# Performance work log

Hardware: AMD Instinct MI355X
Metric: run time of the kernel (lower is better)

The kernel has to match this reference:

```python
import jax, jax.numpy as jnp
import numpy as np

HEADS = 16
SCALE = 8.0
EPS = 1e-12  # F.normalize eps for fp32


def _l2norm(t):
    # F.normalize(t, dim=-1): t / max(||t||, eps)
    n = jnp.sqrt(jnp.sum(t * t, axis=-1, keepdims=True))
    return t / jnp.maximum(n, EPS)


def setup_inputs() -> dict:
    key = jax.random.key(0)
    k0, k1, k2, k3, k4 = jax.random.split(key, 5)
    b, n, d = 1, 4096, 1024
    w_scale = 1.0 / np.sqrt(d)
    return {
        "x": jax.random.normal(k0, (b, n, d), dtype=jnp.float32),
        "Wq": jax.random.normal(k1, (d, d), dtype=jnp.float32) * w_scale,
        "Wk": jax.random.normal(k2, (d, d), dtype=jnp.float32) * w_scale,
        "Wv": jax.random.normal(k3, (d, d), dtype=jnp.float32) * w_scale,
        "Wo": jax.random.normal(k4, (d, d), dtype=jnp.float32) * w_scale,
    }


def reference(x, Wq, Wk, Wv, Wo):
    b, n, d = x.shape
    h = HEADS
    dh = d // h
    # projections (nn.Linear without bias): y = x @ W  (W stored as [in, out])
    def proj(W):
        y = jnp.einsum('bnd,df->bnf', x, W)
        return y.reshape(b, n, h, dh).transpose(0, 2, 1, 3)  # b h n dh
    q, k, v = proj(Wq), proj(Wk), proj(Wv)
    # cosine-sim attention: L2-normalize q, k along head dim
    q = _l2norm(q)
    k = _l2norm(k)
    sim = jnp.einsum('bhid,bhjd->bhij', q, k) * SCALE
    mask_value = -jnp.finfo(sim.dtype).max
    causal = jnp.triu(jnp.ones((n, n), dtype=bool), 1)
    sim = jnp.where(causal, mask_value, sim)
    attn = jax.nn.softmax(sim, axis=-1)
    o = jnp.einsum('bhij,bhjd->bhid', attn, v)
    o = o.transpose(0, 2, 1, 3).reshape(b, n, d)  # b n (h dh)
    return jnp.einsum('bnf,fd->bnd', o, Wo)
```

## Files before the change

kernel.cpp:

```cpp
#include <hip/hip_runtime.h>
#include <stdint.h>
#include <math.h>

typedef __bf16 bf16_t;
typedef __attribute__((ext_vector_type(8))) __bf16 bf16x8;
typedef __attribute__((ext_vector_type(4))) __bf16 bf16x4;
typedef __attribute__((ext_vector_type(4))) float f32x4;

#define N_TOK 4096
#define D_MODEL 1024
#define HEADS 16
#define DH 64
#define C1 11.541560327111707f

__device__ __forceinline__ void async_copy16(const void* g, void* l) {
    __builtin_amdgcn_global_load_lds(
        (const __attribute__((address_space(1))) unsigned int*)g,
        (__attribute__((address_space(3))) unsigned int*)l, 16, 0, 0);
}

__global__ __launch_bounds__(256) void cast_x_kernel(const float* __restrict__ x,
                                                     bf16_t* __restrict__ xb) {
    int i = (blockIdx.x * 256 + threadIdx.x) * 4;
    float4 v = *(const float4*)(x + i);
    bf16x4 o;
    o[0] = (bf16_t)v.x; o[1] = (bf16_t)v.y; o[2] = (bf16_t)v.z; o[3] = (bf16_t)v.w;
    *(bf16x4*)(xb + i) = o;
}

__global__ __launch_bounds__(256) void transpose_w_kernel(
    const float* __restrict__ W0, const float* __restrict__ W1,
    const float* __restrict__ W2, const float* __restrict__ W3,
    bf16_t* __restrict__ T0, bf16_t* __restrict__ T1,
    bf16_t* __restrict__ T2, bf16_t* __restrict__ T3) {
    __shared__ bf16_t t[64][72];
    const float* W; bf16_t* T;
    switch (blockIdx.z) {
        case 0: W = W0; T = T0; break;
        case 1: W = W1; T = T1; break;
        case 2: W = W2; T = T2; break;
        default: W = W3; T = T3; break;
    }
    int k0 = blockIdx.x * 64, n0 = blockIdx.y * 64;
    int tx = threadIdx.x & 63, ty = threadIdx.x >> 6;
#pragma unroll
    for (int i = 0; i < 16; i++) {
        int kl = ty * 16 + i;
        t[kl][tx] = (bf16_t)W[(size_t)(k0 + kl) * D_MODEL + n0 + tx];
    }
    __syncthreads();
#pragma unroll
    for (int i = 0; i < 16; i++) {
        int nl = ty * 16 + i;
        T[(size_t)(n0 + nl) * D_MODEL + k0 + tx] = t[tx][nl];
    }
}

template <int WRITE_F32, int NORM>
__global__ __launch_bounds__(256) void gemm_tile(const bf16_t* __restrict__ A,
                                                 const bf16_t* __restrict__ Bt,
                                                 void* __restrict__ Cout, int ldc) {
    constexpr int K = D_MODEL;
    __shared__ __align__(16) bf16_t As[2][128 * 32];
    __shared__ __align__(16) bf16_t Bs[2][128 * 32];
    const int tid = threadIdx.x;
    const int m0 = blockIdx.y * 128;
    const int n0 = blockIdx.x * 128;
    const int wave = tid >> 6;
    const int lane = tid & 63;
    const int l15 = lane & 15;
    const int quad = lane >> 4;
    const int wm = (wave >> 1) * 64;
    const int wn = (wave & 1) * 64;
    f32x4 acc[4][4] = {};

    const int srow = tid >> 2;
    const int soff = (tid & 3) * 8;
    const bf16_t* gA = A + (size_t)(m0 + srow) * K + soff;
    const bf16_t* gB = Bt + (size_t)(n0 + srow) * K + soff;
    constexpr int HGAP = 64 * K;

    async_copy16(gA, &As[0][tid * 8]);
    async_copy16(gA + HGAP, &As[0][tid * 8 + 2048]);
    async_copy16(gB, &Bs[0][tid * 8]);
    async_copy16(gB + HGAP, &Bs[0][tid * 8 + 2048]);

    for (int kt = 0; kt < K; kt += 32) {
        const int b = (kt >> 5) & 1;
        __syncthreads();
        if (kt + 32 < K) {
            async_copy16(gA + kt + 32, &As[b ^ 1][tid * 8]);
            async_copy16(gA + HGAP + kt + 32, &As[b ^ 1][tid * 8 + 2048]);
            async_copy16(gB + kt + 32, &Bs[b ^ 1][tid * 8]);
            async_copy16(gB + HGAP + kt + 32, &Bs[b ^ 1][tid * 8 + 2048]);
        }
        bf16x8 af[4], bfr[4];
#pragma unroll
        for (int mi = 0; mi < 4; mi++)
            af[mi] = *(const bf16x8*)(&As[b][(wm + mi * 16 + l15) * 32 + quad * 8]);
#pragma unroll
        for (int ni = 0; ni < 4; ni++)
            bfr[ni] = *(const bf16x8*)(&Bs[b][(wn + ni * 16 + l15) * 32 + quad * 8]);
#pragma unroll
        for (int mi = 0; mi < 4; mi++)
#pragma unroll
            for (int ni = 0; ni < 4; ni++)
                acc[mi][ni] = __builtin_amdgcn_mfma_f32_16x16x32_bf16(
                    af[mi], bfr[ni], acc[mi][ni], 0, 0, 0);
    }

    if (NORM && n0 < 2048) {
        const float post = (n0 < 1024) ? C1 : 1.0f;
#pragma unroll
        for (int mi = 0; mi < 4; mi++)
#pragma unroll
            for (int r = 0; r < 4; r++) {
                float s = 0.f;
#pragma unroll
                for (int ni = 0; ni < 4; ni++) {
                    float v = acc[mi][ni][r];
                    s += v * v;
                }
                s += __shfl_xor(s, 1);
                s += __shfl_xor(s, 2);
                s += __shfl_xor(s, 4);
                s += __shfl_xor(s, 8);
                float sc = post / fmaxf(sqrtf(s), 1e-12f);
#pragma unroll
                for (int ni = 0; ni < 4; ni++) acc[mi][ni][r] *= sc;
            }
    }
#pragma unroll
    for (int mi = 0; mi < 4; mi++)
#pragma unroll
        for (int ni = 0; ni < 4; ni++)
#pragma unroll
            for (int r = 0; r < 4; r++) {
                int row = m0 + wm + mi * 16 + quad * 4 + r;
                int col = n0 + wn + ni * 16 + l15;
                float v = acc[mi][ni][r];
                if (WRITE_F32)
                    ((float*)Cout)[(size_t)row * ldc + col] = v;
                else
                    ((bf16_t*)Cout)[(size_t)row * ldc + col] = (bf16_t)v;
            }
}

__global__ __launch_bounds__(256) void transpose_v_kernel(const bf16_t* __restrict__ QKV,
                                                          bf16_t* __restrict__ Vt) {
    __shared__ bf16_t t[64][72];
    int n0 = blockIdx.x * 64;
    int h = blockIdx.y;
    int tx = threadIdx.x & 63, ty = threadIdx.x >> 6;
#pragma unroll
    for (int i = 0; i < 16; i++) {
        int nl = ty * 16 + i;
        t[nl][tx] = QKV[(size_t)(n0 + nl) * 3072 + 2048 + h * DH + tx];
    }
    __syncthreads();
    const int e = tx & 7, q = (tx >> 3) & 3;
    const int J = (tx & 32) + 16 * (e >> 2) + 4 * q + (e & 3);
#pragma unroll
    for (int i = 0; i < 16; i++) {
        int dl = ty * 16 + i;
        Vt[(size_t)(h * DH + dl) * N_TOK + n0 + tx] = t[J][dl];
    }
}

__global__ __launch_bounds__(256) void attn_kernel(const bf16_t* __restrict__ QKV,
                                                   const bf16_t* __restrict__ Vt,
                                                   bf16_t* __restrict__ O) {
    __shared__ __align__(16) bf16_t Ks[2][4096];
    __shared__ __align__(16) bf16_t Vs[2][2][2048];
    const int tid = threadIdx.x;
    const int wave = tid >> 6;
    const int lane = tid & 63;
    const int l15 = lane & 15;
    const int quad = lane >> 4;

    const int xcd = blockIdx.x & 7;
    const int t = blockIdx.x >> 3;
    const int h = xcd * 2 + (t & 1);
    const int u = t >> 1;

    const bf16_t* Qb = QKV + h * DH;
    const bf16_t* Kb = QKV + 1024 + h * DH;
    const bf16_t* Vb = Vt + (size_t)h * DH * N_TOK;

    const int krow = tid >> 3;
    const int kc = (tid & 7) ^ (krow & 7);
    const bf16_t* gK = Kb + (size_t)krow * 3072 + kc * 8;
    const int vd = tid >> 2;
    const int vc = (tid & 3) ^ ((vd >> 1) & 3);
    const bf16_t* gV = Vb + (size_t)vd * N_TOK + vc * 8;

    const int ksw = l15 & 7;
    const int vsw = (l15 >> 1) & 3;

    bf16x8 vone;
#pragma unroll
    for (int i = 0; i < 8; i++) vone[i] = (bf16_t)1.0f;

    for (int ph = 0; ph < 2; ph++) {
        const int g = ph ? u : 63 - u;
        const int i0 = g * 64 + wave * 16;

        bf16x8 aq[2];
#pragma unroll
        for (int kd = 0; kd < 2; kd++)
            aq[kd] = *(const bf16x8*)(Qb + (size_t)(i0 + l15) * 3072 + kd * 32 + quad * 8);

        f32x4 od[4] = {};
        f32x4 lv = {};

        if (ph) __syncthreads();
        async_copy16(gK, &Ks[0][tid * 8]);
        async_copy16(gK + (size_t)32 * 3072, &Ks[0][tid * 8 + 2048]);
        async_copy16(gV, &Vs[0][0][tid * 8]);
        async_copy16(gV + 32, &Vs[0][1][tid * 8]);

        for (int jt = 0; jt <= g; jt++) {
            __syncthreads();
            if (jt < g) {
                const int b = (jt + 1) & 1;
                const bf16_t* kn = gK + (size_t)(jt + 1) * 64 * 3072;
                async_copy16(kn, &Ks[b][tid * 8]);
                async_copy16(kn + (size_t)32 * 3072, &Ks[b][tid * 8 + 2048]);
                async_copy16(gV + (jt + 1) * 64, &Vs[b][0][tid * 8]);
                async_copy16(gV + (jt + 1) * 64 + 32, &Vs[b][1][tid * 8]);
            }
            const bf16_t* KS = Ks[jt & 1];
            const bool diag = (jt == g);
            const int jh_max = diag ? wave : 3;

            bf16x8 ak[4][2];
#pragma unroll
            for (int jh = 0; jh < 4; jh++) {
                if (jh > jh_max) continue;
#pragma unroll
                for (int kd = 0; kd < 2; kd++)
                    ak[jh][kd] = *(const bf16x8*)(&KS[(jh * 16 + l15) * 64 +
                                                      (((kd * 4 + quad) ^ ksw) * 8)]);
            }
            f32x4 sj[4] = {};
#pragma unroll
            for (int kd = 0; kd < 2; kd++)
#pragma unroll
                for (int jh = 0; jh < 4; jh++) {
                    if (jh > jh_max) continue;
                    sj[jh] = __builtin_amdgcn_mfma_f32_16x16x32_bf16(ak[jh][kd], aq[kd], sj[jh], 0, 0, 0);
                }

            float p[4][4] = {};
#pragma unroll
            for (int jh = 0; jh < 4; jh++) {
                if (jh > jh_max) continue;
                if (diag && jh == wave) {
#pragma unroll
                    for (int r = 0; r < 4; r++)
                        p[jh][r] = (quad * 4 + r > l15) ? 0.f
                                   : __builtin_amdgcn_exp2f(sj[jh][r]);
                } else {
#pragma unroll
                    for (int r = 0; r < 4; r++)
                        p[jh][r] = __builtin_amdgcn_exp2f(sj[jh][r]);
                }
            }
            bf16x8 pk8[2];
#pragma unroll
            for (int H = 0; H < 2; H++)
#pragma unroll
                for (int r = 0; r < 4; r++) {
                    pk8[H][r] = (bf16_t)p[2 * H][r];
                    pk8[H][4 + r] = (bf16_t)p[2 * H + 1][r];
                }

            lv = __builtin_amdgcn_mfma_f32_16x16x32_bf16(vone, pk8[0], lv, 0, 0, 0);
            if (jh_max >= 2)
                lv = __builtin_amdgcn_mfma_f32_16x16x32_bf16(vone, pk8[1], lv, 0, 0, 0);

            const bf16_t* VS0 = Vs[jt & 1][0];
#pragma unroll
            for (int mt = 0; mt < 4; mt++) {
                bf16x8 vf = *(const bf16x8*)(&VS0[(mt * 16 + l15) * 32 + ((quad ^ vsw) * 8)]);
                od[mt] = __builtin_amdgcn_mfma_f32_16x16x32_bf16(vf, pk8[0], od[mt], 0, 0, 0);
            }
            if (jh_max >= 2) {
                const bf16_t* VS1 = Vs[jt & 1][1];
#pragma unroll
                for (int mt = 0; mt < 4; mt++) {
                    bf16x8 vf = *(const bf16x8*)(&VS1[(mt * 16 + l15) * 32 + ((quad ^ vsw) * 8)]);
                    od[mt] = __builtin_amdgcn_mfma_f32_16x16x32_bf16(vf, pk8[1], od[mt], 0, 0, 0);
                }
            }
        }

        float inv = 1.0f / lv[0];

#pragma unroll
        for (int mt = 0; mt < 4; mt++) {
            bf16x4 o;
#pragma unroll
            for (int r = 0; r < 4; r++) o[r] = (bf16_t)(od[mt][r] * inv);
            *(bf16x4*)(&O[(size_t)(i0 + l15) * D_MODEL + h * DH + mt * 16 + quad * 4]) = o;
        }
    }
}

extern "C" void kernel_launch(void* const* d_in, const int* in_sizes, int n_in,
                              void* d_out, int out_size, void* d_ws, size_t ws_size,
                              hipStream_t stream) {
    const float* x  = (const float*)d_in[0];
    const float* Wq = (const float*)d_in[1];
    const float* Wk = (const float*)d_in[2];
    const float* Wv = (const float*)d_in[3];
    const float* Wo = (const float*)d_in[4];
    float* out = (float*)d_out;
    char* ws = (char*)d_ws;
    const size_t MB = 1024 * 1024;
    bf16_t* xb   = (bf16_t*)(ws);
    bf16_t* Wt3  = (bf16_t*)(ws + 8 * MB);
    bf16_t* Wot  = (bf16_t*)(ws + 14 * MB);
    bf16_t* QKV  = (bf16_t*)(ws + 16 * MB);
    bf16_t* Vt   = (bf16_t*)(ws + 40 * MB);
    bf16_t* Ob   = (bf16_t*)(ws + 48 * MB);

    cast_x_kernel<<<4096, 256, 0, stream>>>(x, xb);
    dim3 gw(16, 16, 4);
    transpose_w_kernel<<<gw, 256, 0, stream>>>(Wq, Wk, Wv, Wo,
                                               Wt3, Wt3 + 1024 * 1024, Wt3 + 2 * 1024 * 1024, Wot);
    dim3 gqkv(3072 / 128, N_TOK / 128);
    gemm_tile<0, 1><<<gqkv, 256, 0, stream>>>(xb, Wt3, QKV, 3072);
    dim3 gv(N_TOK / 64, HEADS);
    transpose_v_kernel<<<gv, 256, 0, stream>>>(QKV, Vt);
    attn_kernel<<<512, 256, 0, stream>>>(QKV, Vt, Ob);
    dim3 go(D_MODEL / 128, N_TOK / 128);
    gemm_tile<1, 0><<<go, 256, 0, stream>>>(Ob, Wot, out, D_MODEL);
}
```

Before: 203.9 us.

## Split attention key tile across wave pairs with LDS reduction of partial outputs

Each wave now handles 32 query rows against half of the 64-key tile, instead of 16 query rows against all 64 keys. Partial outputs and row sums from the two waves sharing a query group are combined through LDS at the end of each phase. This is meant to reuse each K/V fragment across two query sub-tiles, cutting LDS reads per MFMA and balancing work on the causal diagonal. It costs extra registers, two more barriers, and a reduction step through shared memory.

Result: slower. 221.6 us (+8.7%).

```diff
diff --git a/kernel.cpp b/kernel.cpp
--- a/kernel.cpp
+++ b/kernel.cpp
@@ -177,6 +177,8 @@
     const int lane = tid & 63;
     const int l15 = lane & 15;
     const int quad = lane >> 4;
+    const int qh = wave >> 1;
+    const int H  = wave & 1;
 
     const int xcd = blockIdx.x & 7;
     const int t = blockIdx.x >> 3;
@@ -203,15 +205,18 @@
 
     for (int ph = 0; ph < 2; ph++) {
         const int g = ph ? u : 63 - u;
-        const int i0 = g * 64 + wave * 16;
-
-        bf16x8 aq[2];
-#pragma unroll
-        for (int kd = 0; kd < 2; kd++)
-            aq[kd] = *(const bf16x8*)(Qb + (size_t)(i0 + l15) * 3072 + kd * 32 + quad * 8);
-
-        f32x4 od[4] = {};
-        f32x4 lv = {};
+        const int i_base = g * 64 + qh * 32;
+
+        bf16x8 aq[2][2];
+#pragma unroll
+        for (int s = 0; s < 2; s++)
+#pragma unroll
+            for (int kd = 0; kd < 2; kd++)
+                aq[s][kd] = *(const bf16x8*)(Qb + (size_t)(i_base + s * 16 + l15) * 3072 +
+                                             kd * 32 + quad * 8);
+
+        f32x4 od[2][4] = {};
+        f32x4 lv[2] = {};
 
         if (ph) __syncthreads();
         async_copy16(gK, &Ks[0][tid * 8]);
@@ -231,78 +236,111 @@
             }
             const bf16_t* KS = Ks[jt & 1];
             const bool diag = (jt == g);
-            const int jh_max = diag ? wave : 3;
-
-            bf16x8 ak[4][2];
-#pragma unroll
-            for (int jh = 0; jh < 4; jh++) {
-                if (jh > jh_max) continue;
+
+            bf16x8 ak[2][2];
+#pragma unroll
+            for (int jj = 0; jj < 2; jj++) {
+                if (diag && 2 * H + jj > qh * 2 + 1) continue;
 #pragma unroll
                 for (int kd = 0; kd < 2; kd++)
-                    ak[jh][kd] = *(const bf16x8*)(&KS[(jh * 16 + l15) * 64 +
+                    ak[jj][kd] = *(const bf16x8*)(&KS[((2 * H + jj) * 16 + l15) * 64 +
                                                       (((kd * 4 + quad) ^ ksw) * 8)]);
             }
-            f32x4 sj[4] = {};
+            f32x4 sj[2][2] = {};
 #pragma unroll
             for (int kd = 0; kd < 2; kd++)
 #pragma unroll
-                for (int jh = 0; jh < 4; jh++) {
-                    if (jh > jh_max) continue;
-                    sj[jh] = __builtin_amdgcn_mfma_f32_16x16x32_bf16(ak[jh][kd], aq[kd], sj[jh], 0, 0, 0);
-                }
-
-            float p[4][4] = {};
-#pragma unroll
-            for (int jh = 0; jh < 4; jh++) {
-                if (jh > jh_max) continue;
-                if (diag && jh == wave) {
-#pragma unroll
-                    for (int r = 0; r < 4; r++)
-                        p[jh][r] = (quad * 4 + r > l15) ? 0.f
-                                   : __builtin_amdgcn_exp2f(sj[jh][r]);
-                } else {
-#pragma unroll
-                    for (int r = 0; r < 4; r++)
-                        p[jh][r] = __builtin_amdgcn_exp2f(sj[jh][r]);
-                }
-            }
+                for (int jj = 0; jj < 2; jj++)
+#pragma unroll
+                    for (int s = 0; s < 2; s++) {
+                        if (diag && 2 * H + jj > qh * 2 + s) continue;
+                        sj[s][jj] = __builtin_amdgcn_mfma_f32_16x16x32_bf16(
+                            ak[jj][kd], aq[s][kd], sj[s][jj], 0, 0, 0);
+                    }
+
+            float p[2][2][4] = {};
+#pragma unroll
+            for (int s = 0; s < 2; s++)
+#pragma unroll
+                for (int jj = 0; jj < 2; jj++) {
+                    if (diag && 2 * H + jj > qh * 2 + s) continue;
+                    if (diag && 2 * H + jj == qh * 2 + s) {
+#pragma unroll
+                        for (int r = 0; r < 4; r++)
+                            p[s][jj][r] = (quad * 4 + r > l15) ? 0.f
+                                          : __builtin_amdgcn_exp2f(sj[s][jj][r]);
+                    } else {
+#pragma unroll
+                        for (int r = 0; r < 4; r++)
+                            p[s][jj][r] = __builtin_amdgcn_exp2f(sj[s][jj][r]);
+                    }
+                }
             bf16x8 pk8[2];
 #pragma unroll
-            for (int H = 0; H < 2; H++)
+            for (int s = 0; s < 2; s++)
 #pragma unroll
                 for (int r = 0; r < 4; r++) {
-                    pk8[H][r] = (bf16_t)p[2 * H][r];
-                    pk8[H][4 + r] = (bf16_t)p[2 * H + 1][r];
-                }
-
-            lv = __builtin_amdgcn_mfma_f32_16x16x32_bf16(vone, pk8[0], lv, 0, 0, 0);
-            if (jh_max >= 2)
-                lv = __builtin_amdgcn_mfma_f32_16x16x32_bf16(vone, pk8[1], lv, 0, 0, 0);
-
-            const bf16_t* VS0 = Vs[jt & 1][0];
-#pragma unroll
-            for (int mt = 0; mt < 4; mt++) {
-                bf16x8 vf = *(const bf16x8*)(&VS0[(mt * 16 + l15) * 32 + ((quad ^ vsw) * 8)]);
-                od[mt] = __builtin_amdgcn_mfma_f32_16x16x32_bf16(vf, pk8[0], od[mt], 0, 0, 0);
-            }
-            if (jh_max >= 2) {
-                const bf16_t* VS1 = Vs[jt & 1][1];
+                    pk8[s][r] = (bf16_t)p[s][0][r];
+                    pk8[s][4 + r] = (bf16_t)p[s][1][r];
+                }
+
+            const bool act0 = !(diag && 2 * H > qh * 2);
+            const bool act1 = !(diag && 2 * H > qh * 2 + 1);
+            if (act0 | act1) {
+                const bf16_t* VS = Vs[jt & 1][H];
+                bf16x8 vf[4];
+#pragma unroll
+                for (int mt = 0; mt < 4; mt++)
+                    vf[mt] = *(const bf16x8*)(&VS[(mt * 16 + l15) * 32 + ((quad ^ vsw) * 8)]);
+                if (act0) {
+                    lv[0] = __builtin_amdgcn_mfma_f32_16x16x32_bf16(vone, pk8[0], lv[0], 0, 0, 0);
+#pragma unroll
+                    for (int mt = 0; mt < 4; mt++)
+                        od[0][mt] = __builtin_amdgcn_mfma_f32_16x16x32_bf16(vf[mt], pk8[0], od[0][mt], 0, 0, 0);
+                }
+                if (act1) {
+                    lv[1] = __builtin_amdgcn_mfma_f32_16x16x32_bf16(vone, pk8[1], lv[1], 0, 0, 0);
+#pragma unroll
+                    for (int mt = 0; mt < 4; mt++)
+                        od[1][mt] = __builtin_amdgcn_mfma_f32_16x16x32_bf16(vf[mt], pk8[1], od[1][mt], 0, 0, 0);
+                }
+            }
+        }
+
+        __syncthreads();
+        float* red  = (float*)&Ks[0][0];
+        float* redl = (float*)&Vs[0][0][0];
+        if (H == 1) {
+            const int base = qh * 2048;
+#pragma unroll
+            for (int s = 0; s < 2; s++)
+#pragma unroll
+                for (int mt = 0; mt < 4; mt++)
+                    *(f32x4*)&red[base + (s * 4 + mt) * 256 + lane * 4] = od[s][mt];
+            redl[qh * 128 + lane * 2 + 0] = lv[0][0];
+            redl[qh * 128 + lane * 2 + 1] = lv[1][0];
+        }
+        __syncthreads();
+        if (H == 0) {
+            const int base = qh * 2048;
+            float linv[2];
+#pragma unroll
+            for (int s = 0; s < 2; s++) {
+#pragma unroll
+                for (int mt = 0; mt < 4; mt++)
+                    od[s][mt] += *(const f32x4*)&red[base + (s * 4 + mt) * 256 + lane * 4];
+                linv[s] = 1.0f / (lv[s][0] + redl[qh * 128 + lane * 2 + s]);
+            }
+#pragma unroll
+            for (int s = 0; s < 2; s++)
 #pragma unroll
                 for (int mt = 0; mt < 4; mt++) {
-                    bf16x8 vf = *(const bf16x8*)(&VS1[(mt * 16 + l15) * 32 + ((quad ^ vsw) * 8)]);
-                    od[mt] = __builtin_amdgcn_mfma_f32_16x16x32_bf16(vf, pk8[1], od[mt], 0, 0, 0);
-                }
-            }
-        }
-
-        float inv = 1.0f / lv[0];
-
-#pragma unroll
-        for (int mt = 0; mt < 4; mt++) {
-            bf16x4 o;
-#pragma unroll
-            for (int r = 0; r < 4; r++) o[r] = (bf16_t)(od[mt][r] * inv);
-            *(bf16x4*)(&O[(size_t)(i0 + l15) * D_MODEL + h * DH + mt * 16 + quad * 4]) = o;
+                    bf16x4 o;
+#pragma unroll
+                    for (int r = 0; r < 4; r++) o[r] = (bf16_t)(od[s][mt][r] * linv[s]);
+                    *(bf16x4*)(&O[(size_t)(i_base + s * 16 + l15) * D_MODEL + h * DH +
+                                  mt * 16 + quad * 4]) = o;
+                }
         }
     }
 }
```
